# Performance work log

Hardware: AMD Instinct MI355X
Metric: run time of the kernel (lower is better)

## Reference

```python
import jax, jax.numpy as jnp
import numpy as np
import math

B, H, W, CV = 8, 128, 128, 256
T, CT = 77, 512
HEADS, HEAD_DIM = 8, 32
TOP_M = 5
LN_EPS = 1e-5
NORM_EPS = 1e-6
CLAMP = 2.0


def _ln(x, w, b):
    mu = jnp.mean(x, axis=-1, keepdims=True)
    var = jnp.mean(jnp.square(x - mu), axis=-1, keepdims=True)
    return (x - mu) * jax.lax.rsqrt(var + LN_EPS) * w + b


def _l2norm(x):
    n = jnp.sqrt(jnp.sum(jnp.square(x), axis=-1, keepdims=True))
    return x / jnp.maximum(n, NORM_EPS)


def setup_inputs() -> dict:
    key = jax.random.key(0)
    ks = jax.random.split(key, 12)
    s = 0.02
    return {
        "visual_features": jax.random.normal(ks[0], (B, H, W, CV), jnp.float32),
        "text_features": jax.random.normal(ks[1], (B, T, CT), jnp.float32),
        "norm1_w": jnp.ones((CV,), jnp.float32),
        "norm1_b": jnp.zeros((CV,), jnp.float32),
        "q_w": s * jax.random.normal(ks[2], (CV, CV), jnp.float32),
        "q_b": jnp.zeros((CV,), jnp.float32),
        "k_w": s * jax.random.normal(ks[3], (CT, CV), jnp.float32),
        "k_b": jnp.zeros((CV,), jnp.float32),
        "v_w": s * jax.random.normal(ks[4], (CT, CV), jnp.float32),
        "v_b": jnp.zeros((CV,), jnp.float32),
        "out_w": s * jax.random.normal(ks[5], (CV, CV), jnp.float32),
        "out_b": jnp.zeros((CV,), jnp.float32),
        "gate_w": s * jax.random.normal(ks[6], (CV, 1), jnp.float32),
        "gate_b": jnp.zeros((1,), jnp.float32),
        "logit_scale": jnp.asarray(math.log(1.0 / 0.07), jnp.float32),
        "alpha": jnp.asarray(0.1, jnp.float32),
        "norm2_w": jnp.ones((CV,), jnp.float32),
        "norm2_b": jnp.zeros((CV,), jnp.float32),
        "ffn1_w": s * jax.random.normal(ks[7], (CV, 4 * CV), jnp.float32),
        "ffn1_b": jnp.zeros((4 * CV,), jnp.float32),
        "ffn2_w": s * jax.random.normal(ks[8], (4 * CV, CV), jnp.float32),
        "ffn2_b": jnp.zeros((CV,), jnp.float32),
    }


def reference(visual_features, text_features, norm1_w, norm1_b, q_w, q_b, k_w, k_b,
              v_w, v_b, out_w, out_b, gate_w, gate_b, logit_scale, alpha,
              norm2_w, norm2_b, ffn1_w, ffn1_b, ffn2_w, ffn2_b):
    b, h, w, cv = visual_features.shape
    n = h * w
    # Pre-LN then flatten spatial dims: (B, N, Cv)
    x = _ln(visual_features, norm1_w, norm1_b).reshape(b, n, cv)
    q_full = x @ q_w + q_b                      # (B, N, Cv)
    k_full = text_features @ k_w + k_b          # (B, T, Cv)
    v_full = text_features @ v_w + v_b          # (B, T, Cv)
    # padding mask: all-zero text tokens
    pad = jnp.sum(jnp.abs(text_features), axis=-1) <= 1e-6  # (B, T)
    # cosine-normalize over FULL Cv dim, then split heads
    q = _l2norm(q_full).reshape(b, n, HEADS, HEAD_DIM)
    k = _l2norm(k_full).reshape(b, -1, HEADS, HEAD_DIM)
    v = v_full.reshape(b, -1, HEADS, HEAD_DIM)
    scale = jnp.exp(jnp.clip(logit_scale, -CLAMP, CLAMP)) / jnp.sqrt(jnp.float32(HEAD_DIM))
    sim = jnp.einsum('bnhd,bthd->bnht', q, k) * scale  # (B, N, Hh, T)
    sim = jnp.where(pad[:, None, None, :], -jnp.inf, sim)
    # top-k pruning over text tokens (threshold at k-th value; ties measure-zero)
    topv = jax.lax.top_k(sim, TOP_M)[0]
    sim = jnp.where(sim >= topv[..., -1:], sim, -jnp.inf)
    attn = jax.nn.softmax(sim, axis=-1)
    aligned = jnp.einsum('bnht,bthd->bnhd', attn, v).reshape(b, n, cv)
    aligned = aligned @ out_w + out_b
    gate = jax.nn.sigmoid(x @ gate_w + gate_b)  # (B, N, 1)
    y = x + alpha * gate * aligned
    y = _ln(y, norm2_w, norm2_b)
    ffn = jax.nn.gelu(y @ ffn1_w + ffn1_b, approximate=False) @ ffn2_w + ffn2_b
    y = y + ffn
    return y.reshape(b, h, w, cv)
```

## Files before the change

### kernel.cpp

```cpp
#include <hip/hip_runtime.h>
#include <hip/hip_bf16.h>

typedef _Float16 h16;
typedef __attribute__((ext_vector_type(8))) _Float16 halfx8;
typedef __attribute__((ext_vector_type(4))) _Float16 halfx4;
typedef __attribute__((ext_vector_type(4))) float f32x4;

__device__ __forceinline__ void gload_lds16(const void* g, void* l) {
  __builtin_amdgcn_global_load_lds((const __attribute__((address_space(1))) unsigned int*)g,
                                   (__attribute__((address_space(3))) unsigned int*)l, 16, 0, 0);
}
__device__ __forceinline__ unsigned umax_(unsigned a, unsigned b) { return a > b ? a : b; }
__device__ __forceinline__ unsigned umin_(unsigned a, unsigned b) { return a < b ? a : b; }

__device__ __forceinline__ float fast_gelu(float v) {
  float x2 = v * v;
  float w_ = v * fmaf(x2, 0.0713548163f, 1.5957691216f);
  float e = __expf(w_);
  float r = 1.f / (1.f + e);
  return v * e * r;
}

__global__ __launch_bounds__(256) void conv_all_kernel(
    const float* __restrict__ qw, const float* __restrict__ ow,
    const float* __restrict__ f1w, const float* __restrict__ f2w,
    h16* __restrict__ qwT, h16* __restrict__ owT,
    h16* __restrict__ f1T, h16* __restrict__ f2T)
{
  int bid = blockIdx.x, tid = threadIdx.x;
  const float* in; h16* out; int logN, K, base;
  if (bid < 256)       { in = qw;  out = qwT; logN = 8;  K = 256;  base = 0; }
  else if (bid < 512)  { in = ow;  out = owT; logN = 8;  K = 256;  base = 256; }
  else if (bid < 1536) { in = f1w; out = f1T; logN = 10; K = 256;  base = 512; }
  else                 { in = f2w; out = f2T; logN = 8;  K = 1024; base = 1536; }
  int idx = (bid - base) * 256 + tid;
  int k = idx >> logN, n = idx & ((1 << logN) - 1);
  out[(size_t)n * K + k] = (h16)in[idx];
}

__global__ __launch_bounds__(256) void text_kv_kernel(const float* __restrict__ tf,
    const float* __restrict__ kw, const float* __restrict__ kb,
    const float* __restrict__ vw, const float* __restrict__ vb,
    const float* __restrict__ lsp,
    h16* __restrict__ ko, h16* __restrict__ vo, float* __restrict__ padf)
{
  __shared__ h16 st[4 * 512];
  __shared__ float kro[4 * 256];
  __shared__ float ssc[4];
  int bx = blockIdx.x, b = bx / 20, tg = bx % 20, t0 = tg * 4;
  int tid = threadIdx.x, lane = tid & 63, wid = tid >> 6;
  for (int i = tid; i < 4 * 512; i += 256) {
    int tl = i >> 9, j = i & 511, t = t0 + tl;
    float v = (t < 77) ? tf[((size_t)b * 77 + t) * 512 + j] : 0.f;
    st[i] = (h16)v;
  }
  __syncthreads();
  {
    int t = t0 + wid;
    float a = 0.f;
    #pragma unroll
    for (int j = 0; j < 8; j++) a += fabsf((float)st[wid * 512 + lane + j * 64]);
    #pragma unroll
    for (int o = 32; o; o >>= 1) a += __shfl_xor(a, o);
    if (lane == 0) padf[b * 80 + t] = (a <= 1e-6f) ? -1e30f : 0.f;
  }
  int c = tid;
  float kacc[4], vacc[4];
  #pragma unroll
  for (int tl = 0; tl < 4; tl++) { kacc[tl] = kb[c]; vacc[tl] = vb[c]; }
  for (int j = 0; j < 512; j++) {
    float wkv = kw[(size_t)j * 256 + c];
    float wvv = vw[(size_t)j * 256 + c];
    #pragma unroll
    for (int tl = 0; tl < 4; tl++) {
      float x = (float)st[tl * 512 + j];
      kacc[tl] += x * wkv; vacc[tl] += x * wvv;
    }
  }
  #pragma unroll
  for (int tl = 0; tl < 4; tl++) kro[tl * 256 + c] = kacc[tl] * kacc[tl];
  __syncthreads();
  {
    float s2 = kro[wid * 256 + lane] + kro[wid * 256 + lane + 64]
             + kro[wid * 256 + lane + 128] + kro[wid * 256 + lane + 192];
    #pragma unroll
    for (int o = 32; o; o >>= 1) s2 += __shfl_xor(s2, o);
    if (lane == 0) {
      float ls = lsp[0];
      float scale = __expf(fminf(fmaxf(ls, -2.f), 2.f)) * rsqrtf(32.f);
      ssc[wid] = scale / fmaxf(sqrtf(s2), 1e-6f);
    }
  }
  __syncthreads();
  int h = c >> 5, d = c & 31, g = d >> 3, e = d & 7;
  #pragma unroll
  for (int tl = 0; tl < 4; tl++) {
    int t = t0 + tl;
    int kt = t >> 4, l15 = t & 15, ln = g * 16 + l15;
    size_t koff = ((((size_t)(b * 8 + h) * 5 + kt) * 64) + ln) * 8 + e;
    size_t voff = (((size_t)(b * 8 + h) * 80) + t) * 32 + d;
    ko[koff] = (t < 77) ? (h16)(kacc[tl] * ssc[tl]) : (h16)0.f;
    vo[voff] = (t < 77) ? (h16)vacc[tl] : (h16)0.f;
  }
}

__global__ __launch_bounds__(256) void ln1_kernel(const float* __restrict__ vis,
    const float* __restrict__ w, const float* __restrict__ bia,
    const float* __restrict__ gw, const float* __restrict__ gb,
    h16* __restrict__ x, float* __restrict__ gate)
{
  int lane = threadIdx.x & 63;
  size_t row = (size_t)blockIdx.x * 4 + (threadIdx.x >> 6);
  const float4 v = ((const float4*)(vis + row * 256))[lane];
  float s = v.x + v.y + v.z + v.w;
  float q = v.x * v.x + v.y * v.y + v.z * v.z + v.w * v.w;
  #pragma unroll
  for (int o = 32; o; o >>= 1) { s += __shfl_xor(s, o); q += __shfl_xor(q, o); }
  float mean = s * (1.f / 256.f);
  float rstd = rsqrtf(q * (1.f / 256.f) - mean * mean + 1e-5f);
  float4 wv = ((const float4*)w)[lane], bv = ((const float4*)bia)[lane];
  float x0 = (v.x - mean) * rstd * wv.x + bv.x;
  float x1 = (v.y - mean) * rstd * wv.y + bv.y;
  float x2 = (v.z - mean) * rstd * wv.z + bv.z;
  float x3 = (v.w - mean) * rstd * wv.w + bv.w;
  float4 gv = ((const float4*)gw)[lane];
  float g = x0 * gv.x + x1 * gv.y + x2 * gv.z + x3 * gv.w;
  #pragma unroll
  for (int o = 32; o; o >>= 1) g += __shfl_xor(g, o);
  if (lane == 0) gate[row] = 1.f / (1.f + __expf(-(g + gb[0])));
  halfx4 o4; o4[0] = (h16)x0; o4[1] = (h16)x1; o4[2] = (h16)x2; o4[3] = (h16)x3;
  ((halfx4*)(x + row * 256))[lane] = o4;
}

__global__ __launch_bounds__(256) void gemmQ_kernel(const h16* __restrict__ A,
    const h16* __restrict__ Wt, const float* __restrict__ bias, h16* __restrict__ outp)
{
  __shared__ char sA[8192];
  __shared__ char sB[32768];
  int m0 = blockIdx.x * 64;
  int tid = threadIdx.x, lane = tid & 63, wid = tid >> 6;
  int wn = wid;
  int l15 = lane & 15, l4 = lane >> 4, xk = l15 & 7;
  f32x4 acc[4][4];
  #pragma unroll
  for (int a = 0; a < 4; a++)
    #pragma unroll
    for (int b2 = 0; b2 < 4; b2++) acc[a][b2] = (f32x4){0.f, 0.f, 0.f, 0.f};
  const size_t sa = 512;
  int srow = lane >> 3;
  int scol = ((lane & 7) ^ srow) * 16;
  const char* Ab = (const char*)A + (size_t)m0 * sa + scol;
  const char* Bb = (const char*)Wt + scol;
  for (int k0 = 0; k0 < 256; k0 += 64) {
    #pragma unroll
    for (int cc = 0; cc < 2; cc++) {
      int ch = wid * 2 + cc;
      gload_lds16(Ab + (size_t)(ch * 8 + srow) * sa + k0 * 2, sA + ch * 1024);
    }
    #pragma unroll
    for (int cc = 0; cc < 8; cc++) {
      int ch = wid * 8 + cc;
      gload_lds16(Bb + (size_t)(ch * 8 + srow) * sa + k0 * 2, sB + ch * 1024);
    }
    asm volatile("s_waitcnt vmcnt(0)" ::: "memory");
    __syncthreads();
    #pragma unroll
    for (int ks = 0; ks < 2; ks++) {
      halfx8 af[4], bf[4];
      #pragma unroll
      for (int f = 0; f < 4; f++) {
        af[f] = *(const halfx8*)(sA + (f * 16 + l15) * 128 + (((ks * 4 + l4) ^ xk) * 16));
        bf[f] = *(const halfx8*)(sB + (wn * 64 + f * 16 + l15) * 128 + (((ks * 4 + l4) ^ xk) * 16));
      }
      #pragma unroll
      for (int fm = 0; fm < 4; fm++)
        #pragma unroll
        for (int fn = 0; fn < 4; fn++)
          acc[fm][fn] = __builtin_amdgcn_mfma_f32_16x16x32_f16(af[fm], bf[fn], acc[fm][fn], 0, 0, 0);
    }
    __syncthreads();
  }
  float bv[4];
  #pragma unroll
  for (int fn = 0; fn < 4; fn++) bv[fn] = bias[wn * 64 + fn * 16 + l15];
  float ps[4][4];
  #pragma unroll
  for (int fm = 0; fm < 4; fm++)
    #pragma unroll
    for (int r = 0; r < 4; r++) {
      float s = 0.f;
      #pragma unroll
      for (int fn = 0; fn < 4; fn++) {
        float v = acc[fm][fn][r] + bv[fn];
        acc[fm][fn][r] = v;
        s += v * v;
      }
      ps[fm][r] = s;
    }
  #pragma unroll
  for (int o = 1; o <= 8; o <<= 1)
    #pragma unroll
    for (int fm = 0; fm < 4; fm++)
      #pragma unroll
      for (int r = 0; r < 4; r++) ps[fm][r] += __shfl_xor(ps[fm][r], o);
  if (l15 == 0) {
    #pragma unroll
    for (int fm = 0; fm < 4; fm++)
      #pragma unroll
      for (int r = 0; r < 4; r++)
        ((float*)sA)[(fm * 16 + l4 * 4 + r) * 4 + wn] = ps[fm][r];
  }
  __syncthreads();
  #pragma unroll
  for (int fm = 0; fm < 4; fm++)
    #pragma unroll
    for (int r = 0; r < 4; r++) {
      const float* p = (const float*)sA + (fm * 16 + l4 * 4 + r) * 4;
      float S = p[0] + p[1] + p[2] + p[3];
      float sc = 1.f / fmaxf(sqrtf(S), 1e-6f);
      size_t row = (size_t)(m0 + fm * 16 + l4 * 4 + r);
      #pragma unroll
      for (int fn = 0; fn < 4; fn++)
        outp[row * 256 + wn * 64 + fn * 16 + l15] = (h16)(acc[fm][fn][r] * sc);
    }
}

__global__ __launch_bounds__(256) void gemmO_kernel(const h16* __restrict__ A,
    const h16* __restrict__ Wt, const float* __restrict__ ob,
    const h16* __restrict__ x, const float* __restrict__ gate,
    const float* __restrict__ alphap, const float* __restrict__ w2,
    const float* __restrict__ b2, h16* __restrict__ outp)
{
  __shared__ char sA[8192];
  __shared__ char sB[32768];
  int m0 = blockIdx.x * 64;
  int tid = threadIdx.x, lane = tid & 63, wid = tid >> 6;
  int wn = wid;
  int l15 = lane & 15, l4 = lane >> 4, xk = l15 & 7;
  f32x4 acc[4][4];
  #pragma unroll
  for (int a = 0; a < 4; a++)
    #pragma unroll
    for (int b2_ = 0; b2_ < 4; b2_++) acc[a][b2_] = (f32x4){0.f, 0.f, 0.f, 0.f};
  const size_t sa = 512;
  int srow = lane >> 3;
  int scol = ((lane & 7) ^ srow) * 16;
  const char* Ab = (const char*)A + (size_t)m0 * sa + scol;
  const char* Bb = (const char*)Wt + scol;
  for (int k0 = 0; k0 < 256; k0 += 64) {
    #pragma unroll
    for (int cc = 0; cc < 2; cc++) {
      int ch = wid * 2 + cc;
      gload_lds16(Ab + (size_t)(ch * 8 + srow) * sa + k0 * 2, sA + ch * 1024);
    }
    #pragma unroll
    for (int cc = 0; cc < 8; cc++) {
      int ch = wid * 8 + cc;
      gload_lds16(Bb + (size_t)(ch * 8 + srow) * sa + k0 * 2, sB + ch * 1024);
    }
    asm volatile("s_waitcnt vmcnt(0)" ::: "memory");
    __syncthreads();
    #pragma unroll
    for (int ks = 0; ks < 2; ks++) {
      halfx8 af[4], bf[4];
      #pragma unroll
      for (int f = 0; f < 4; f++) {
        af[f] = *(const halfx8*)(sA + (f * 16 + l15) * 128 + (((ks * 4 + l4) ^ xk) * 16));
        bf[f] = *(const halfx8*)(sB + (wn * 64 + f * 16 + l15) * 128 + (((ks * 4 + l4) ^ xk) * 16));
      }
      #pragma unroll
      for (int fm = 0; fm < 4; fm++)
        #pragma unroll
        for (int fn = 0; fn < 4; fn++)
          acc[fm][fn] = __builtin_amdgcn_mfma_f32_16x16x32_f16(af[fm], bf[fn], acc[fm][fn], 0, 0, 0);
    }
    __syncthreads();
  }
  float bv[4], w2v[4], b2v[4];
  #pragma unroll
  for (int fn = 0; fn < 4; fn++) {
    int col = wn * 64 + fn * 16 + l15;
    bv[fn] = ob[col]; w2v[fn] = w2[col]; b2v[fn] = b2[col];
  }
  float al = alphap[0];
  float s1[4][4], s2[4][4];
  #pragma unroll
  for (int fm = 0; fm < 4; fm++)
    #pragma unroll
    for (int r = 0; r < 4; r++) {
      size_t row = (size_t)(m0 + fm * 16 + l4 * 4 + r);
      float ga = al * gate[row];
      float a1 = 0.f, a2 = 0.f;
      #pragma unroll
      for (int fn = 0; fn < 4; fn++) {
        float v = acc[fm][fn][r] + bv[fn];
        float xv = (float)x[row * 256 + wn * 64 + fn * 16 + l15];
        float y = xv + ga * v;
        acc[fm][fn][r] = y;
        a1 += y; a2 += y * y;
      }
      s1[fm][r] = a1; s2[fm][r] = a2;
    }
  #pragma unroll
  for (int o = 1; o <= 8; o <<= 1)
    #pragma unroll
    for (int fm = 0; fm < 4; fm++)
      #pragma unroll
      for (int r = 0; r < 4; r++) {
        s1[fm][r] += __shfl_xor(s1[fm][r], o);
        s2[fm][r] += __shfl_xor(s2[fm][r], o);
      }
  if (l15 == 0) {
    #pragma unroll
    for (int fm = 0; fm < 4; fm++)
      #pragma unroll
      for (int r = 0; r < 4; r++) {
        int rr = fm * 16 + l4 * 4 + r;
        ((float*)sA)[rr * 8 + wn * 2 + 0] = s1[fm][r];
        ((float*)sA)[rr * 8 + wn * 2 + 1] = s2[fm][r];
      }
  }
  __syncthreads();
  #pragma unroll
  for (int fm = 0; fm < 4; fm++)
    #pragma unroll
    for (int r = 0; r < 4; r++) {
      int rr = fm * 16 + l4 * 4 + r;
      const float* p = (const float*)sA + rr * 8;
      float S1 = p[0] + p[2] + p[4] + p[6];
      float S2 = p[1] + p[3] + p[5] + p[7];
      float mean = S1 * (1.f / 256.f);
      float var = S2 * (1.f / 256.f) - mean * mean;
      float rstd = rsqrtf(var + 1e-5f);
      size_t row = (size_t)(m0 + rr);
      #pragma unroll
      for (int fn = 0; fn < 4; fn++) {
        float y = acc[fm][fn][r];
        outp[row * 256 + wn * 64 + fn * 16 + l15] =
            (h16)((y - mean) * rstd * w2v[fn] + b2v[fn]);
      }
    }
}

__device__ __forceinline__ void ffn_stage_w1(const h16* __restrict__ w1t,
                                             int c, char* dW1, int tid, int wid)
{
  #pragma unroll
  for (int j = 0; j < 4; j++) {
    int i = j * 512 + tid;
    int r = i >> 5, g = i & 31;
    gload_lds16(w1t + (size_t)(c * 64 + r) * 256 + ((g ^ (r & 7)) * 8),
                dW1 + (j * 512 + wid * 64) * 16);
  }
}
__device__ __forceinline__ void ffn_stage_w2(const h16* __restrict__ w2t,
                                             int c, char* dW2, int tid, int wid)
{
  #pragma unroll
  for (int j = 0; j < 4; j++) {
    int i = j * 512 + tid;
    int r = i >> 3, g = i & 7;
    gload_lds16(w2t + (size_t)r * 1024 + c * 64 + ((g ^ (r & 7)) * 8),
                dW2 + (j * 512 + wid * 64) * 16);
  }
}

__global__ __launch_bounds__(512, 2) void ffn_fused_kernel(
    const h16* __restrict__ y2g, const h16* __restrict__ w1t, const float* __restrict__ b1,
    const h16* __restrict__ w2t, const float* __restrict__ b2, float* __restrict__ outp)
{
  __shared__ char smem[163840];
  float* sE = (float*)smem;

  int m0 = blockIdx.x * 128;
  int tid = threadIdx.x, lane = tid & 63, wid = tid >> 6;
  int l15 = lane & 15, l4 = lane >> 4;
  int wm1 = wid >> 1, wn1 = wid & 1;
  int wm2 = wid >> 2, wn2 = wid & 3;

  halfx8 afy[2][8];
  #pragma unroll
  for (int fm = 0; fm < 2; fm++) {
    size_t row = (size_t)(m0 + wm1 * 32 + fm * 16 + l15);
    #pragma unroll
    for (int ks = 0; ks < 8; ks++)
      afy[fm][ks] = *(const halfx8*)&y2g[row * 256 + ks * 32 + l4 * 8];
  }

  f32x4 acc2[4][4];
  #pragma unroll
  for (int a = 0; a < 4; a++)
    #pragma unroll
    for (int b_ = 0; b_ < 4; b_++) acc2[a][b_] = (f32x4){0.f, 0.f, 0.f, 0.f};

  ffn_stage_w1(w1t, 0, smem, tid, wid);
  float b1v0 = b1[wn1 * 32 + l15];
  float b1v1 = b1[wn1 * 32 + 16 + l15];
  asm volatile("s_waitcnt vmcnt(0)" ::: "memory");
  __builtin_amdgcn_s_barrier();
  asm volatile("" ::: "memory");

  for (int c = 0; c < 16; c++) {
    int buf = c & 1;
    char* sW1c = smem + buf * 32768;
    if (c < 15) ffn_stage_w1(w1t, c + 1, smem + (buf ^ 1) * 32768, tid, wid);
    ffn_stage_w2(w2t, c, smem + 65536 + buf * 32768, tid, wid);
    float nb0 = 0.f, nb1 = 0.f;
    if (c < 15) {
      nb0 = b1[(c + 1) * 64 + wn1 * 32 + l15];
      nb1 = b1[(c + 1) * 64 + wn1 * 32 + 16 + l15];
    }

    f32x4 a1[2][2];
    #pragma unroll
    for (int a = 0; a < 2; a++)
      #pragma unroll
      for (int b_ = 0; b_ < 2; b_++) a1[a][b_] = (f32x4){0.f, 0.f, 0.f, 0.f};
    __builtin_amdgcn_s_setprio(1);
    #pragma unroll
    for (int ks = 0; ks < 8; ks++) {
      #pragma unroll
      for (int fc = 0; fc < 2; fc++) {
        int nrow = wn1 * 32 + fc * 16 + l15;
        halfx8 bf = *(const halfx8*)(sW1c + (size_t)nrow * 512 + (((ks * 4 + l4) ^ (nrow & 7)) * 16));
        #pragma unroll
        for (int fm = 0; fm < 2; fm++)
          a1[fm][fc] = __builtin_amdgcn_mfma_f32_16x16x32_f16(afy[fm][ks], bf, a1[fm][fc], 0, 0, 0);
      }
    }
    __builtin_amdgcn_s_setprio(0);

    {
      char* sHc = smem + 131072 + buf * 16384;
      #pragma unroll
      for (int fm = 0; fm < 2; fm++)
        #pragma unroll
        for (int fc = 0; fc < 2; fc++)
          #pragma unroll
          for (int r = 0; r < 4; r++) {
            int row = wm1 * 32 + fm * 16 + l4 * 4 + r;
            int col = wn1 * 32 + fc * 16 + l15;
            float v = fast_gelu(a1[fm][fc][r] + (fc ? b1v1 : b1v0));
            ((h16*)(sHc + row * 128 + (((col >> 3) ^ (row & 7)) * 16)))[col & 7] = (h16)v;
          }
    }

    if (c > 0) {
      char* sHp = smem + 131072 + (buf ^ 1) * 16384;
      char* sW2p = smem + 65536 + (buf ^ 1) * 32768;
      __builtin_amdgcn_s_setprio(1);
      #pragma unroll
      for (int ks = 0; ks < 2; ks++) {
        halfx8 ah[4], bw[4];
        #pragma unroll
        for (int f = 0; f < 4; f++) {
          int hrow = wm2 * 64 + f * 16 + l15;
          ah[f] = *(const halfx8*)(sHp + hrow * 128 + (((ks * 4 + l4) ^ (hrow & 7)) * 16));
          int wrow = wn2 * 64 + f * 16 + l15;
          bw[f] = *(const halfx8*)(sW2p + (size_t)wrow * 128 + (((ks * 4 + l4) ^ (wrow & 7)) * 16));
        }
        #pragma unroll
        for (int fm = 0; fm < 4; fm++)
          #pragma unroll
          for (int fn = 0; fn < 4; fn++)
            acc2[fm][fn] = __builtin_amdgcn_mfma_f32_16x16x32_f16(ah[fm], bw[fn], acc2[fm][fn], 0, 0, 0);
      }
      __builtin_amdgcn_s_setprio(0);
    }

    asm volatile("s_waitcnt lgkmcnt(0)" ::: "memory");
    asm volatile("s_waitcnt vmcnt(0)" ::: "memory");
    __builtin_amdgcn_s_barrier();
    asm volatile("" ::: "memory");
    b1v0 = nb0; b1v1 = nb1;
  }

  {
    char* sHp = smem + 131072 + 16384;
    char* sW2p = smem + 65536 + 32768;
    __builtin_amdgcn_s_setprio(1);
    #pragma unroll
    for (int ks = 0; ks < 2; ks++) {
      halfx8 ah[4], bw[4];
      #pragma unroll
      for (int f = 0; f < 4; f++) {
        int hrow = wm2 * 64 + f * 16 + l15;
        ah[f] = *(const halfx8*)(sHp + hrow * 128 + (((ks * 4 + l4) ^ (hrow & 7)) * 16));
        int wrow = wn2 * 64 + f * 16 + l15;
        bw[f] = *(const halfx8*)(sW2p + (size_t)wrow * 128 + (((ks * 4 + l4) ^ (wrow & 7)) * 16));
      }
      #pragma unroll
      for (int fm = 0; fm < 4; fm++)
        #pragma unroll
        for (int fn = 0; fn < 4; fn++)
          acc2[fm][fn] = __builtin_amdgcn_mfma_f32_16x16x32_f16(ah[fm], bw[fn], acc2[fm][fn], 0, 0, 0);
    }
    __builtin_amdgcn_s_setprio(0);
  }

  int rowl = tid >> 3, cg = tid & 7;
  #pragma unroll
  for (int half = 0; half < 2; half++) {
    if (wm2 == half) {
      #pragma unroll
      for (int fm = 0; fm < 4; fm++)
        #pragma unroll
        for (int fn = 0; fn < 4; fn++)
          #pragma unroll
          for (int r = 0; r < 4; r++)
            sE[(fm * 16 + l4 * 4 + r) * 264 + wn2 * 64 + fn * 16 + l15] = acc2[fm][fn][r];
    }
    __syncthreads();
    size_t grow = (size_t)(m0 + half * 64 + rowl);
    #pragma unroll
    for (int k = 0; k < 8; k++) {
      int c0 = cg * 4 + k * 32;
      float4 v = *(float4*)&sE[rowl * 264 + c0];
      halfx4 rv = *(const halfx4*)&y2g[grow * 256 + c0];
      float4 bb = *(const float4*)&b2[c0];
      float4 o;
      o.x = v.x + (float)rv[0] + bb.x;
      o.y = v.y + (float)rv[1] + bb.y;
      o.z = v.z + (float)rv[2] + bb.z;
      o.w = v.w + (float)rv[3] + bb.w;
      *(float4*)&outp[grow * 256 + c0] = o;
    }
    __syncthreads();
  }
}

__global__ __launch_bounds__(256) void attn_kernel(const h16* __restrict__ q,
    const h16* __restrict__ kk,
    const h16* __restrict__ vv,
    const float* __restrict__ padf,
    h16* __restrict__ outp)
{
  int bx = blockIdx.x;
  int wid = threadIdx.x >> 6, lane = threadIdx.x & 63;
  int l15 = lane & 15, g = lane >> 4;
  int b = bx >> 8;
  size_t qrow = (size_t)bx * 64 + wid * 16 + l15;
  int base4 = g * 4;
  float pad4[5][4];
  #pragma unroll
  for (int kt = 0; kt < 5; kt++) {
    float4 p4 = *(const float4*)&padf[b * 80 + kt * 16 + base4];
    pad4[kt][0] = p4.x; pad4[kt][1] = p4.y; pad4[kt][2] = p4.z; pad4[kt][3] = p4.w;
  }
  const h16* qp = &q[qrow * 256 + g * 8];
  h16* op = &outp[qrow * 256 + g * 8];
  #pragma unroll 2
  for (int h = 0; h < 8; h++) {
    int ho = h * 32;
    halfx8 qf = *(const halfx8*)(qp + ho);
    const h16* kph = kk + (((size_t)(b * 8 + h) * 5) * 64 + lane) * 8;
    const h16* vph = vv + ((size_t)(b * 8 + h) * 80) * 32 + g * 8;
    f32x4 acc[5];
    #pragma unroll
    for (int kt = 0; kt < 5; kt++) {
      halfx8 kf = *(const halfx8*)(kph + kt * 512);
      acc[kt] = __builtin_amdgcn_mfma_f32_16x16x32_f16(kf, qf, (f32x4){0.f, 0.f, 0.f, 0.f}, 0, 0, 0);
    }
    unsigned pv0 = 0u, pv1 = 0u, pv2 = 0u, pv3 = 0u, pv4 = 0u;
    #pragma unroll
    for (int kt = 0; kt < 5; kt++) {
      #pragma unroll
      for (int r = 0; r < 4; r++) {
        float s = acc[kt][r] + pad4[kt][r];
        int bi = __float_as_int(s);
        unsigned u = ((unsigned)(bi ^ ((bi >> 31) | (int)0x80000000)) & 0xFFFFFF80u)
                   | (unsigned)(base4 + kt * 16 + r);
        unsigned a;
        a = umax_(pv0, u); u = umin_(pv0, u); pv0 = a;
        a = umax_(pv1, u); u = umin_(pv1, u); pv1 = a;
        a = umax_(pv2, u); u = umin_(pv2, u); pv2 = a;
        a = umax_(pv3, u); u = umin_(pv3, u); pv3 = a;
        pv4 = umax_(pv4, u);
      }
    }
    #pragma unroll
    for (int mrd = 0; mrd < 2; mrd++) {
      int msk = mrd ? 32 : 16;
      unsigned b0 = (unsigned)__shfl_xor((int)pv0, msk);
      unsigned b1 = (unsigned)__shfl_xor((int)pv1, msk);
      unsigned b2 = (unsigned)__shfl_xor((int)pv2, msk);
      unsigned b3 = (unsigned)__shfl_xor((int)pv3, msk);
      unsigned b4 = (unsigned)__shfl_xor((int)pv4, msk);
      unsigned c0 = umax_(pv0, b0);
      unsigned c1 = umax_(umax_(umin_(pv0, b0), pv1), b1);
      unsigned c2 = umax_(umax_(umin_(pv0, b1), umin_(pv1, b0)), umax_(pv2, b2));
      unsigned c3 = umax_(umax_(umax_(umin_(pv0, b2), umin_(pv1, b1)), umin_(pv2, b0)), umax_(pv3, b3));
      unsigned c4 = umax_(umax_(umax_(umin_(pv0, b3), umin_(pv1, b2)),
                                umax_(umin_(pv2, b1), umin_(pv3, b0))), umax_(pv4, b4));
      pv0 = c0; pv1 = c1; pv2 = c2; pv3 = c3; pv4 = c4;
    }
    unsigned pvs[5] = {pv0, pv1, pv2, pv3, pv4};
    float pw[5]; int ti[5]; float den = 0.f;
    #pragma unroll
    for (int k = 0; k < 5; k++) {
      unsigned u = pvs[k];
      int sg = ((int)u) >> 31;
      float tv = __int_as_float(u ^ (0x80000000u | (unsigned)~sg));
      ti[k] = (int)(u & 0x7Fu);
      pw[k] = __expf(tv);
      den += pw[k];
    }
    float inv = 1.f / den;
    halfx8 o8 = {};
    #pragma unroll
    for (int k = 0; k < 5; k++) {
      h16 ph = (h16)(pw[k] * inv);
      halfx8 v = *(const halfx8*)(vph + ti[k] * 32);
      halfx8 p8 = {ph, ph, ph, ph, ph, ph, ph, ph};
      o8 = o8 + p8 * v;
    }
    *(halfx8*)(op + ho) = o8;
  }
}

extern "C" void kernel_launch(void* const* d_in, const int* in_sizes, int n_in,
                              void* d_out, int out_size, void* d_ws, size_t ws_size,
                              hipStream_t stream)
{
  const float* vis = (const float*)d_in[0];
  const float* tf  = (const float*)d_in[1];
  const float* n1w = (const float*)d_in[2];
  const float* n1b = (const float*)d_in[3];
  const float* qw  = (const float*)d_in[4];
  const float* qb  = (const float*)d_in[5];
  const float* kw  = (const float*)d_in[6];
  const float* kb  = (const float*)d_in[7];
  const float* vw  = (const float*)d_in[8];
  const float* vb  = (const float*)d_in[9];
  const float* ow  = (const float*)d_in[10];
  const float* ob  = (const float*)d_in[11];
  const float* gw  = (const float*)d_in[12];
  const float* gb  = (const float*)d_in[13];
  const float* ls  = (const float*)d_in[14];
  const float* al  = (const float*)d_in[15];
  const float* n2w = (const float*)d_in[16];
  const float* n2b = (const float*)d_in[17];
  const float* f1w = (const float*)d_in[18];
  const float* f1b = (const float*)d_in[19];
  const float* f2w = (const float*)d_in[20];
  const float* f2b = (const float*)d_in[21];

  char* ws = (char*)d_ws;
  const size_t MB_ = 1024ull * 1024ull;
  h16*  kS   = (h16*)(ws + 0 * MB_);
  h16*  vS   = (h16*)(ws + 1 * MB_);
  float* padf = (float*)(ws + 2 * MB_);
  float* gate = (float*)(ws + 3 * MB_);
  h16*  qwT  = (h16*)(ws + 4 * MB_);
  h16*  owT  = (h16*)(ws + 5 * MB_);
  h16*  f1T  = (h16*)(ws + 6 * MB_);
  h16*  f2T  = (h16*)(ws + 7 * MB_);
  h16*  xh   = (h16*)(ws + 16 * MB_);
  h16*  qh   = (h16*)(ws + 80 * MB_);
  h16*  alg  = (h16*)(ws + 144 * MB_);

  conv_all_kernel<<<2560, 256, 0, stream>>>(qw, ow, f1w, f2w, qwT, owT, f1T, f2T);

  text_kv_kernel<<<160, 256, 0, stream>>>(tf, kw, kb, vw, vb, ls, kS, vS, padf);
  ln1_kernel<<<32768, 256, 0, stream>>>(vis, n1w, n1b, gw, gb, xh, gate);

  gemmQ_kernel<<<2048, 256, 0, stream>>>(xh, qwT, qb, qh);

  attn_kernel<<<2048, 256, 0, stream>>>(qh, kS, vS, padf, qh);

  gemmO_kernel<<<2048, 256, 0, stream>>>(qh, owT, ob, xh, gate, al, n2w, n2b, alg);

  ffn_fused_kernel<<<1024, 512, 0, stream>>>(alg, f1T, f1b, f2T, f2b, (float*)d_out);
}
```

Measured before the change: 544.3 us.

## Fuse Q projection GEMM with top-k attention via LDS-staged normalized Q

```diff
diff --git a/kernel.cpp b/kernel.cpp
--- a/kernel.cpp
+++ b/kernel.cpp
@@ -132,8 +132,12 @@
   ((halfx4*)(x + row * 256))[lane] = o4;
 }
 
-__global__ __launch_bounds__(256) void gemmQ_kernel(const h16* __restrict__ A,
-    const h16* __restrict__ Wt, const float* __restrict__ bias, h16* __restrict__ outp)
+__global__ __launch_bounds__(256) void gemmQA_kernel(const h16* __restrict__ A,
+    const h16* __restrict__ Wt, const float* __restrict__ bias,
+    const h16* __restrict__ kk,
+    const h16* __restrict__ vv,
+    const float* __restrict__ padf,
+    h16* __restrict__ outp)
 {
   __shared__ char sA[8192];
   __shared__ char sB[32768];
@@ -218,11 +222,99 @@
       const float* p = (const float*)sA + (fm * 16 + l4 * 4 + r) * 4;
       float S = p[0] + p[1] + p[2] + p[3];
       float sc = 1.f / fmaxf(sqrtf(S), 1e-6f);
-      size_t row = (size_t)(m0 + fm * 16 + l4 * 4 + r);
-      #pragma unroll
-      for (int fn = 0; fn < 4; fn++)
-        outp[row * 256 + wn * 64 + fn * 16 + l15] = (h16)(acc[fm][fn][r] * sc);
-    }
+      int row = fm * 16 + l4 * 4 + r;
+      #pragma unroll
+      for (int fn = 0; fn < 4; fn++) {
+        int col = wn * 64 + fn * 16 + l15;
+        ((h16*)(sB + row * 512 + (((col >> 3) ^ (row & 7)) * 16)))[col & 7] =
+            (h16)(acc[fm][fn][r] * sc);
+      }
+    }
+  __syncthreads();
+
+  {
+    int bx = blockIdx.x;
+    int g = l4;
+    int b = bx >> 8;
+    size_t qrow = (size_t)bx * 64 + wid * 16 + l15;
+    int base4 = g * 4;
+    float pad4[5][4];
+    #pragma unroll
+    for (int kt = 0; kt < 5; kt++) {
+      float4 p4 = *(const float4*)&padf[b * 80 + kt * 16 + base4];
+      pad4[kt][0] = p4.x; pad4[kt][1] = p4.y; pad4[kt][2] = p4.z; pad4[kt][3] = p4.w;
+    }
+    const char* qsrc = sB + (wid * 16 + l15) * 512;
+    int rk = l15 & 7;
+    h16* op = &outp[qrow * 256 + g * 8];
+    #pragma unroll 2
+    for (int h = 0; h < 8; h++) {
+      int ho = h * 32;
+      halfx8 qf = *(const halfx8*)(qsrc + (((h * 4 + l4) ^ rk) * 16));
+      const h16* kph = kk + (((size_t)(b * 8 + h) * 5) * 64 + lane) * 8;
+      const h16* vph = vv + ((size_t)(b * 8 + h) * 80) * 32 + g * 8;
+      f32x4 acc5[5];
+      #pragma unroll
+      for (int kt = 0; kt < 5; kt++) {
+        halfx8 kf = *(const halfx8*)(kph + kt * 512);
+        acc5[kt] = __builtin_amdgcn_mfma_f32_16x16x32_f16(kf, qf, (f32x4){0.f, 0.f, 0.f, 0.f}, 0, 0, 0);
+      }
+      unsigned pv0 = 0u, pv1 = 0u, pv2 = 0u, pv3 = 0u, pv4 = 0u;
+      #pragma unroll
+      for (int kt = 0; kt < 5; kt++) {
+        #pragma unroll
+        for (int r = 0; r < 4; r++) {
+          float s = acc5[kt][r] + pad4[kt][r];
+          int bi = __float_as_int(s);
+          unsigned u = ((unsigned)(bi ^ ((bi >> 31) | (int)0x80000000)) & 0xFFFFFF80u)
+                     | (unsigned)(base4 + kt * 16 + r);
+          unsigned a;
+          a = umax_(pv0, u); u = umin_(pv0, u); pv0 = a;
+          a = umax_(pv1, u); u = umin_(pv1, u); pv1 = a;
+          a = umax_(pv2, u); u = umin_(pv2, u); pv2 = a;
+          a = umax_(pv3, u); u = umin_(pv3, u); pv3 = a;
+          pv4 = umax_(pv4, u);
+        }
+      }
+      #pragma unroll
+      for (int mrd = 0; mrd < 2; mrd++) {
+        int msk = mrd ? 32 : 16;
+        unsigned b0 = (unsigned)__shfl_xor((int)pv0, msk);
+        unsigned b1 = (unsigned)__shfl_xor((int)pv1, msk);
+        unsigned b2 = (unsigned)__shfl_xor((int)pv2, msk);
+        unsigned b3 = (unsigned)__shfl_xor((int)pv3, msk);
+        unsigned b4 = (unsigned)__shfl_xor((int)pv4, msk);
+        unsigned c0 = umax_(pv0, b0);
+        unsigned c1 = umax_(umax_(umin_(pv0, b0), pv1), b1);
+        unsigned c2 = umax_(umax_(umin_(pv0, b1), umin_(pv1, b0)), umax_(pv2, b2));
+        unsigned c3 = umax_(umax_(umax_(umin_(pv0, b2), umin_(pv1, b1)), umin_(pv2, b0)), umax_(pv3, b3));
+        unsigned c4 = umax_(umax_(umax_(umin_(pv0, b3), umin_(pv1, b2)),
+                                  umax_(umin_(pv2, b1), umin_(pv3, b0))), umax_(pv4, b4));
+        pv0 = c0; pv1 = c1; pv2 = c2; pv3 = c3; pv4 = c4;
+      }
+      unsigned pvs[5] = {pv0, pv1, pv2, pv3, pv4};
+      float pw[5]; int ti[5]; float den = 0.f;
+      #pragma unroll
+      for (int k = 0; k < 5; k++) {
+        unsigned u = pvs[k];
+        int sg = ((int)u) >> 31;
+        float tv = __int_as_float(u ^ (0x80000000u | (unsigned)~sg));
+        ti[k] = (int)(u & 0x7Fu);
+        pw[k] = __expf(tv);
+        den += pw[k];
+      }
+      float inv = 1.f / den;
+      halfx8 o8 = {};
+      #pragma unroll
+      for (int k = 0; k < 5; k++) {
+        h16 ph = (h16)(pw[k] * inv);
+        halfx8 v = *(const halfx8*)(vph + ti[k] * 32);
+        halfx8 p8 = {ph, ph, ph, ph, ph, ph, ph, ph};
+        o8 = o8 + p8 * v;
+      }
+      *(halfx8*)(op + ho) = o8;
+    }
+  }
 }
 
 __global__ __launch_bounds__(256) void gemmO_kernel(const h16* __restrict__ A,
@@ -526,95 +618,6 @@
       *(float4*)&outp[grow * 256 + c0] = o;
     }
     __syncthreads();
-  }
-}
-
-__global__ __launch_bounds__(256) void attn_kernel(const h16* __restrict__ q,
-    const h16* __restrict__ kk,
-    const h16* __restrict__ vv,
-    const float* __restrict__ padf,
-    h16* __restrict__ outp)
-{
-  int bx = blockIdx.x;
-  int wid = threadIdx.x >> 6, lane = threadIdx.x & 63;
-  int l15 = lane & 15, g = lane >> 4;
-  int b = bx >> 8;
-  size_t qrow = (size_t)bx * 64 + wid * 16 + l15;
-  int base4 = g * 4;
-  float pad4[5][4];
-  #pragma unroll
-  for (int kt = 0; kt < 5; kt++) {
-    float4 p4 = *(const float4*)&padf[b * 80 + kt * 16 + base4];
-    pad4[kt][0] = p4.x; pad4[kt][1] = p4.y; pad4[kt][2] = p4.z; pad4[kt][3] = p4.w;
-  }
-  const h16* qp = &q[qrow * 256 + g * 8];
-  h16* op = &outp[qrow * 256 + g * 8];
-  #pragma unroll 2
-  for (int h = 0; h < 8; h++) {
-    int ho = h * 32;
-    halfx8 qf = *(const halfx8*)(qp + ho);
-    const h16* kph = kk + (((size_t)(b * 8 + h) * 5) * 64 + lane) * 8;
-    const h16* vph = vv + ((size_t)(b * 8 + h) * 80) * 32 + g * 8;
-    f32x4 acc[5];
-    #pragma unroll
-    for (int kt = 0; kt < 5; kt++) {
-      halfx8 kf = *(const halfx8*)(kph + kt * 512);
-      acc[kt] = __builtin_amdgcn_mfma_f32_16x16x32_f16(kf, qf, (f32x4){0.f, 0.f, 0.f, 0.f}, 0, 0, 0);
-    }
-    unsigned pv0 = 0u, pv1 = 0u, pv2 = 0u, pv3 = 0u, pv4 = 0u;
-    #pragma unroll
-    for (int kt = 0; kt < 5; kt++) {
-      #pragma unroll
-      for (int r = 0; r < 4; r++) {
-        float s = acc[kt][r] + pad4[kt][r];
-        int bi = __float_as_int(s);
-        unsigned u = ((unsigned)(bi ^ ((bi >> 31) | (int)0x80000000)) & 0xFFFFFF80u)
-                   | (unsigned)(base4 + kt * 16 + r);
-        unsigned a;
-        a = umax_(pv0, u); u = umin_(pv0, u); pv0 = a;
-        a = umax_(pv1, u); u = umin_(pv1, u); pv1 = a;
-        a = umax_(pv2, u); u = umin_(pv2, u); pv2 = a;
-        a = umax_(pv3, u); u = umin_(pv3, u); pv3 = a;
-        pv4 = umax_(pv4, u);
-      }
-    }
-    #pragma unroll
-    for (int mrd = 0; mrd < 2; mrd++) {
-      int msk = mrd ? 32 : 16;
-      unsigned b0 = (unsigned)__shfl_xor((int)pv0, msk);
-      unsigned b1 = (unsigned)__shfl_xor((int)pv1, msk);
-      unsigned b2 = (unsigned)__shfl_xor((int)pv2, msk);
-      unsigned b3 = (unsigned)__shfl_xor((int)pv3, msk);
-      unsigned b4 = (unsigned)__shfl_xor((int)pv4, msk);
-      unsigned c0 = umax_(pv0, b0);
-      unsigned c1 = umax_(umax_(umin_(pv0, b0), pv1), b1);
-      unsigned c2 = umax_(umax_(umin_(pv0, b1), umin_(pv1, b0)), umax_(pv2, b2));
-      unsigned c3 = umax_(umax_(umax_(umin_(pv0, b2), umin_(pv1, b1)), umin_(pv2, b0)), umax_(pv3, b3));
-      unsigned c4 = umax_(umax_(umax_(umin_(pv0, b3), umin_(pv1, b2)),
-                                umax_(umin_(pv2, b1), umin_(pv3, b0))), umax_(pv4, b4));
-      pv0 = c0; pv1 = c1; pv2 = c2; pv3 = c3; pv4 = c4;
-    }
-    unsigned pvs[5] = {pv0, pv1, pv2, pv3, pv4};
-    float pw[5]; int ti[5]; float den = 0.f;
-    #pragma unroll
-    for (int k = 0; k < 5; k++) {
-      unsigned u = pvs[k];
-      int sg = ((int)u) >> 31;
-      float tv = __int_as_float(u ^ (0x80000000u | (unsigned)~sg));
-      ti[k] = (int)(u & 0x7Fu);
-      pw[k] = __expf(tv);
-      den += pw[k];
-    }
-    float inv = 1.f / den;
-    halfx8 o8 = {};
-    #pragma unroll
-    for (int k = 0; k < 5; k++) {
-      h16 ph = (h16)(pw[k] * inv);
-      halfx8 v = *(const halfx8*)(vph + ti[k] * 32);
-      halfx8 p8 = {ph, ph, ph, ph, ph, ph, ph, ph};
-      o8 = o8 + p8 * v;
-    }
-    *(halfx8*)(op + ho) = o8;
   }
 }
 
@@ -664,9 +667,7 @@
   text_kv_kernel<<<160, 256, 0, stream>>>(tf, kw, kb, vw, vb, ls, kS, vS, padf);
   ln1_kernel<<<32768, 256, 0, stream>>>(vis, n1w, n1b, gw, gb, xh, gate);
 
-  gemmQ_kernel<<<2048, 256, 0, stream>>>(xh, qwT, qb, qh);
-
-  attn_kernel<<<2048, 256, 0, stream>>>(qh, kS, vS, padf, qh);
+  gemmQA_kernel<<<2048, 256, 0, stream>>>(xh, qwT, qb, kS, vS, padf, qh);
 
   gemmO_kernel<<<2048, 256, 0, stream>>>(qh, owT, ob, xh, gate, al, n2w, n2b, alg);
 
```

After: 523.9 us. 1.04x faster.
